# Kernel tuning notes

Measured on AMD Instinct MI355X. Metric: run time of the kernel, lower is better.

## Reference

```python
import jax, jax.numpy as jnp
import numpy as np

N_NODES = 100000
N_EDGES = 1600000
NEG_SLOPE = 0.2


def gat_layer(x, edge_index, W, att_src, att_dst, bias, concat):
    """PyG-style GATConv (v1) with self-loops added, dropout=0."""
    N = x.shape[0]
    H, C = att_src.shape
    ar = jnp.arange(N)
    src = jnp.concatenate([edge_index[0], ar])  # add self-loops
    dst = jnp.concatenate([edge_index[1], ar])
    h = (x @ W).reshape(N, H, C)                # [N,H,C]
    a_src = jnp.sum(h * att_src[None], axis=-1)  # [N,H]
    a_dst = jnp.sum(h * att_dst[None], axis=-1)  # [N,H]
    e = jax.nn.leaky_relu(a_src[src] + a_dst[dst], NEG_SLOPE)  # [E,H]
    # segment softmax over destination nodes
    m = jax.ops.segment_max(e, dst, num_segments=N)
    e = jnp.exp(e - m[dst])
    s = jax.ops.segment_sum(e, dst, num_segments=N)
    alpha = e / (s[dst] + 1e-16)                # [E,H]
    msg = h[src] * alpha[:, :, None]            # [E,H,C]
    out = jax.ops.segment_sum(msg, dst, num_segments=N)  # [N,H,C]
    if concat:
        out = out.reshape(N, H * C)
    else:
        out = out.mean(axis=1)
    return out + bias


def prelu(x, a):
    return jnp.where(x >= 0, x, a * x)


def setup_inputs() -> dict:
    key = jax.random.key(0)
    ks = jax.random.split(key, 12)
    def g(k, shape, fan):
        return jax.random.normal(k, shape, dtype=jnp.float32) * (1.0 / np.sqrt(fan))
    x = jax.random.normal(ks[0], (N_NODES, 256), dtype=jnp.float32)
    edge_index = jax.random.randint(ks[1], (2, N_EDGES), 0, N_NODES, dtype=jnp.int64 if jax.config.read('jax_enable_x64') else jnp.int32)
    return {
        'x': x,
        'edge_index': edge_index,
        'W1': g(ks[2], (256, 64), 256), 'as1': g(ks[3], (8, 8), 8), 'ad1': g(ks[4], (8, 8), 8), 'b1': jnp.zeros((64,), jnp.float32),
        'W2': g(ks[5], (320, 64), 320), 'as2': g(ks[6], (8, 8), 8), 'ad2': g(ks[7], (8, 8), 8), 'b2': jnp.zeros((64,), jnp.float32),
        'W3': g(ks[8], (64, 128), 64), 'as3': g(ks[9], (8, 16), 16), 'ad3': g(ks[10], (8, 16), 16), 'b3': jnp.zeros((16,), jnp.float32),
        'p1': jnp.full((1,), 0.25, jnp.float32), 'p2': jnp.full((1,), 0.25, jnp.float32),
    }


def reference(x, edge_index, W1, as1, ad1, b1, W2, as2, ad2, b2, W3, as3, ad3, b3, p1, p2):
    h = gat_layer(x, edge_index, W1, as1, ad1, b1, concat=True)
    h = prelu(h, p1)
    h = gat_layer(jnp.concatenate([x, h], axis=1), edge_index, W2, as2, ad2, b2, concat=True)
    h = prelu(h, p2)
    h = gat_layer(h, edge_index, W3, as3, ad3, b3, concat=False)
    return jax.nn.log_softmax(h, axis=1)
```

## Files before the change

kernel.cpp:

```cpp
#include <hip/hip_runtime.h>
#include <hip/hip_bf16.h>
#include <stdint.h>

typedef unsigned short u16;
typedef __attribute__((ext_vector_type(8))) short short8;
typedef __attribute__((ext_vector_type(8))) __bf16 bf16x8;
typedef __attribute__((ext_vector_type(4))) float f32x4;
typedef __attribute__((ext_vector_type(4))) float fv4;

#define DEV static __device__ __forceinline__

DEV float bf2f(u16 u) { uint32_t i = ((uint32_t)u) << 16; float f; __builtin_memcpy(&f, &i, 4); return f; }
DEV u16 f2bf(float f) {
    uint32_t i; __builtin_memcpy(&i, &f, 4);
    uint32_t r = i + 0x7FFFu + ((i >> 16) & 1u);
    return (u16)(r >> 16);
}
DEV float lo16f(uint32_t u) { uint32_t i = u << 16; float f; __builtin_memcpy(&f, &i, 4); return f; }
DEV float hi16f(uint32_t u) { uint32_t i = u & 0xFFFF0000u; float f; __builtin_memcpy(&f, &i, 4); return f; }
DEV uint32_t pack2(float a, float b) { return (uint32_t)f2bf(a) | ((uint32_t)f2bf(b) << 16); }
DEV float lrelu(float x) { return x >= 0.f ? x : 0.2f * x; }

#define CHK 4096
#define BN2SH 10
#define BN2 1024

__global__ __launch_bounds__(256) void k_cvt(const float* __restrict__ in, u16* __restrict__ out, int n4) {
    int i = blockIdx.x * 256 + threadIdx.x;
    if (i < n4) {
        fv4 v = __builtin_nontemporal_load((const fv4*)in + i);
        uint64_t o = (uint64_t)f2bf(v.x) | ((uint64_t)f2bf(v.y) << 16)
                   | ((uint64_t)f2bf(v.z) << 32) | ((uint64_t)f2bf(v.w) << 48);
        __builtin_nontemporal_store(o, (uint64_t*)out + i);
    }
}

__global__ __launch_bounds__(256) void k_wt(const float* __restrict__ W, u16* __restrict__ out, int K, int M) {
    int i = blockIdx.x * 256 + threadIdx.x;
    int nko = K >> 3;
    int total = (M >> 6) * 64 * nko;
    if (i >= total) return;
    int c = i % nko;
    int m = (i / nko) & 63;
    int cb = i / (nko * 64);
    const float* wp = W + (size_t)(c * 8) * M + cb * 64 + m;
    uint64_t w0 = (uint64_t)f2bf(wp[0])
                | ((uint64_t)f2bf(wp[(size_t)M]) << 16)
                | ((uint64_t)f2bf(wp[(size_t)2 * M]) << 32)
                | ((uint64_t)f2bf(wp[(size_t)3 * M]) << 48);
    uint64_t w1 = (uint64_t)f2bf(wp[(size_t)4 * M])
                | ((uint64_t)f2bf(wp[(size_t)5 * M]) << 16)
                | ((uint64_t)f2bf(wp[(size_t)6 * M]) << 32)
                | ((uint64_t)f2bf(wp[(size_t)7 * M]) << 48);
    uint64_t* d = (uint64_t*)out + (size_t)i * 2;
    d[0] = w0; d[1] = w1;
}

__global__ __launch_bounds__(256) void k_hist(const int* __restrict__ dst, int* __restrict__ hist,
                                              int NBUK, int nbp, int E) {
    __shared__ int h[BN2];
    int tid = threadIdx.x;
    for (int i = tid; i < NBUK; i += 256) h[i] = 0;
    __syncthreads();
    int b0 = blockIdx.x * CHK;
    int jend = b0 + CHK < E ? b0 + CHK : E;
    for (int j = b0 + tid; j < jend; j += 256)
        atomicAdd(&h[dst[j] >> BN2SH], 1);
    __syncthreads();
    for (int i = tid; i < NBUK; i += 256) hist[i * nbp + blockIdx.x] = h[i];
}

__global__ void k_scanpart(const int* __restrict__ deg, int* __restrict__ bsum, int n) {
    __shared__ int buf[1024];
    int tid = threadIdx.x;
    int i = blockIdx.x * 1024 + tid;
    int v = (i < n) ? deg[i] : 0;
    buf[tid] = v; __syncthreads();
    for (int d = 512; d > 0; d >>= 1) {
        if (tid < d) buf[tid] += buf[tid + d];
        __syncthreads();
    }
    if (tid == 0) bsum[blockIdx.x] = buf[0];
}

__global__ void k_scanbsum(int* bsum, int nb) {
    if (threadIdx.x == 0) {
        int run = 0;
        for (int b = 0; b < nb; ++b) { int t = bsum[b]; bsum[b] = run; run += t; }
    }
}

__global__ void k_scanonly(const int* __restrict__ in, const int* __restrict__ bsum,
                           int* __restrict__ out, int n) {
    __shared__ int buf[1024];
    int tid = threadIdx.x;
    int i = blockIdx.x * 1024 + tid;
    int v = (i < n) ? in[i] : 0;
    buf[tid] = v; __syncthreads();
    for (int d = 1; d < 1024; d <<= 1) {
        int t = (tid >= d) ? buf[tid - d] : 0;
        __syncthreads();
        buf[tid] += t;
        __syncthreads();
    }
    if (i < n) out[i] = buf[tid] - v + bsum[blockIdx.x];
}

__global__ __launch_bounds__(256) void k_part(const int* __restrict__ src, const int* __restrict__ dst,
                                              const int* __restrict__ scanned, int* __restrict__ stage,
                                              int NBUK, int nbp, int E) {
    __shared__ int cur[BN2];
    int tid = threadIdx.x;
    for (int i = tid; i < NBUK; i += 256) cur[i] = scanned[i * nbp + blockIdx.x];
    __syncthreads();
    int b0 = blockIdx.x * CHK;
    int jend = b0 + CHK < E ? b0 + CHK : E;
    for (int j = b0 + tid; j < jend; j += 256) {
        int d = dst[j];
        int p = atomicAdd(&cur[d >> BN2SH], 1);
        stage[p] = src[j] | ((d & (BN2 - 1)) << 17);
    }
}

__global__ __launch_bounds__(256) void k_csr(const int* __restrict__ stage, const int* __restrict__ scanned,
                                             int* __restrict__ off, int* __restrict__ srt,
                                             int NBUK, int nbp, int N, int E) {
    __shared__ int deg[BN2];
    __shared__ int ex[BN2];
    __shared__ int tsum[256];
    int tid = threadIdx.x, b = blockIdx.x;
    int base = b << BN2SH;
    int s0 = scanned[b * nbp];
    int s1 = (b + 1 < NBUK) ? scanned[(b + 1) * nbp] : E;
    for (int i = tid; i < BN2; i += 256) deg[i] = 0;
    __syncthreads();
    for (int j = s0 + tid; j < s1; j += 256) atomicAdd(&deg[(uint32_t)stage[j] >> 17], 1);
    __syncthreads();
    int t4 = tid * 4;
    int d0 = deg[t4], d1 = deg[t4 + 1], d2 = deg[t4 + 2], d3 = deg[t4 + 3];
    int tot = d0 + d1 + d2 + d3;
    tsum[tid] = tot; __syncthreads();
    for (int d = 1; d < 256; d <<= 1) {
        int t = (tid >= d) ? tsum[tid - d] : 0;
        __syncthreads();
        tsum[tid] += t;
        __syncthreads();
    }
    int ebase = tsum[tid] - tot;
    ex[t4] = ebase; ex[t4 + 1] = ebase + d0; ex[t4 + 2] = ebase + d0 + d1; ex[t4 + 3] = ebase + d0 + d1 + d2;
    __syncthreads();
    for (int i = tid; i < BN2; i += 256) { int n = base + i; if (n < N) off[n] = s0 + ex[i]; }
    if (b == 0 && tid == 0) off[N] = E;
    __syncthreads();
    for (int j = s0 + tid; j < s1; j += 256) {
        int sd = stage[j];
        int p = atomicAdd(&ex[(uint32_t)sd >> 17], 1);
        srt[s0 + p] = sd & 0x1FFFF;
    }
}

__global__ __launch_bounds__(256) void gemm_k(const u16* __restrict__ A1, int K1,
                                              const u16* __restrict__ A2, int K2,
                                              const u16* __restrict__ wbt, int M,
                                              u16* __restrict__ out, int N,
                                              const float* __restrict__ ats, const float* __restrict__ atd,
                                              float* __restrict__ a_src, float* __restrict__ a_dst, int hs) {
    __shared__ u16 wt2[40][64][8];
    const int K = K1 + K2;
    const int nc = K >> 3;
    const int tid = threadIdx.x;
    const int n0 = blockIdx.x * 64;
    const int cb = blockIdx.y * 64;

    const u16* wB = wbt + (size_t)cb * K;
    for (int p = tid; p < (nc << 6); p += 256) {
        int c = p >> 6, m = p & 63;
        *(int4*)&wt2[c][m][0] = *(const int4*)(wB + (size_t)m * K + c * 8);
    }
    __syncthreads();

    const int wv = tid >> 6, lane = tid & 63;
    const int quad = lane >> 4, r = lane & 15;
    f32x4 acc[4];
#pragma unroll
    for (int ct = 0; ct < 4; ++ct) acc[ct] = (f32x4){0.f, 0.f, 0.f, 0.f};

    int arow = n0 + wv * 16 + r;
    int ar = arow < N ? arow : N - 1;
    const u16* rowA1 = A1 + (size_t)ar * K1;
    const u16* rowA2 = A2 ? (A2 + (size_t)ar * K2 - K1) : rowA1;

    const int nit = K >> 5;
    for (int it = 0; it < nit; ++it) {
        int kk = (it << 5) + quad * 8;
        const u16* ap = (kk < K1) ? (rowA1 + kk) : (rowA2 + kk);
        bf16x8 a = __builtin_bit_cast(bf16x8, *(const short8*)ap);
        int cbase = it << 2;
#pragma unroll
        for (int ct = 0; ct < 4; ++ct) {
            bf16x8 b = __builtin_bit_cast(bf16x8, *(const short8*)&wt2[cbase + quad][ct * 16 + r][0]);
            acc[ct] = __builtin_amdgcn_mfma_f32_16x16x32_bf16(a, b, acc[ct], 0, 0, 0);
        }
    }

    const int rmask = (1 << hs) - 1;
#pragma unroll
    for (int ct = 0; ct < 4; ++ct) {
        int col = cb + ct * 16 + r;
        float as_c = ats[col];
        float ad_c = atd[col];
#pragma unroll
        for (int rg = 0; rg < 4; ++rg) {
            int grow = n0 + wv * 16 + quad * 4 + rg;
            float p = acc[ct][rg];
            if (grow < N) out[(size_t)grow * M + col] = f2bf(p);
            float ps = p * as_c;
            float pd = p * ad_c;
            ps += __shfl_xor(ps, 1); pd += __shfl_xor(pd, 1);
            ps += __shfl_xor(ps, 2); pd += __shfl_xor(pd, 2);
            ps += __shfl_xor(ps, 4); pd += __shfl_xor(pd, 4);
            if (rmask == 15) { ps += __shfl_xor(ps, 8); pd += __shfl_xor(pd, 8); }
            if ((r & rmask) == 0 && grow < N) {
                int head = col >> hs;
                a_src[grow * 8 + head] = ps;
                a_dst[grow * 8 + head] = pd;
            }
        }
    }
}

__global__ __launch_bounds__(256) void agg12(const u16* __restrict__ g,
                                             const float* __restrict__ a_src, const float* __restrict__ a_dst,
                                             const int* __restrict__ off, const int* __restrict__ srt,
                                             const float* __restrict__ bias, const float* __restrict__ pslope,
                                             u16* __restrict__ hout, int N) {
    int tid = threadIdx.x;
    int lane32 = tid & 31;
    int node = blockIdx.x * 8 + (tid >> 5);
    int nd = node < N ? node : N - 1;
    int lane16 = lane32 & 15;
    int sub    = lane32 >> 4;
    int hg     = lane16 >> 1;
    int hw     = lane32 & 7;
    int e4     = lane32 >> 3;
    const char* gb = (const char*)g;

    float ad_acc = a_dst[nd * 8 + hg];
    float ad_w   = a_dst[nd * 8 + hw];
    float ws = __expf(lrelu(a_src[nd * 8 + hg] + ad_acc));
    float m0 = (sub == 0) ? ws : 0.f;
    uint2 gs = *(const uint2*)(gb + ((size_t)nd << 7) + lane16 * 8);
    float s = m0;
    float acc0 = m0 * lo16f(gs.x), acc1 = m0 * hi16f(gs.x);
    float acc2 = m0 * lo16f(gs.y), acc3 = m0 * hi16f(gs.y);

    int jb = off[nd], je = off[nd + 1];
    int addrH = (tid & 32) * 4;
    int addrS = addrH + sub * 32;
    int addrW = addrS + hg * 4;
    int laneoff = lane16 * 8;

    int idx = 0; float asv = 0.f;
    if (jb < je) {
        int jc = jb + e4; jc = jc < je ? jc : je - 1;
        idx = srt[jc];
        asv = a_src[idx * 8 + hw];
    }
    for (int j = jb; j < je; j += 4) {
        float w = __expf(lrelu(asv + ad_w));
        w = (j + e4 < je) ? w : 0.f;
        int wi = __builtin_bit_cast(int, w);
        int jn = j + 4 + e4; jn = jn < je ? jn : je - 1;
        int idx_n = srt[jn];
        float as_n = a_src[idx_n * 8 + hw];

        int sv0 = __builtin_amdgcn_ds_bpermute(addrS,      idx);
        int wb0 = __builtin_amdgcn_ds_bpermute(addrW,      wi);
        int sv1 = __builtin_amdgcn_ds_bpermute(addrS + 64, idx);
        int wb1 = __builtin_amdgcn_ds_bpermute(addrW + 64, wi);
        uint2 g0 = *(const uint2*)(gb + (((uint32_t)sv0 << 7) + laneoff));
        uint2 g1 = *(const uint2*)(gb + (((uint32_t)sv1 << 7) + laneoff));
        float wv0 = __builtin_bit_cast(float, wb0);
        float wv1 = __builtin_bit_cast(float, wb1);
        s += wv0;
        acc0 += wv0 * lo16f(g0.x); acc1 += wv0 * hi16f(g0.x);
        acc2 += wv0 * lo16f(g0.y); acc3 += wv0 * hi16f(g0.y);
        s += wv1;
        acc0 += wv1 * lo16f(g1.x); acc1 += wv1 * hi16f(g1.x);
        acc2 += wv1 * lo16f(g1.y); acc3 += wv1 * hi16f(g1.y);
        idx = idx_n; asv = as_n;
    }
    s    += __shfl_xor(s,    16);
    acc0 += __shfl_xor(acc0, 16); acc1 += __shfl_xor(acc1, 16);
    acc2 += __shfl_xor(acc2, 16); acc3 += __shfl_xor(acc3, 16);
    if (node < N && sub == 0) {
        float r = 1.f / (s + 1e-16f);
        fv4 bv = *(const fv4*)(bias + lane16 * 4);
        float p = pslope[0];
        float v0 = acc0 * r + bv.x; v0 = v0 >= 0.f ? v0 : p * v0;
        float v1 = acc1 * r + bv.y; v1 = v1 >= 0.f ? v1 : p * v1;
        float v2 = acc2 * r + bv.z; v2 = v2 >= 0.f ? v2 : p * v2;
        float v3 = acc3 * r + bv.w; v3 = v3 >= 0.f ? v3 : p * v3;
        uint2 o; o.x = pack2(v0, v1); o.y = pack2(v2, v3);
        *(uint2*)((char*)hout + ((size_t)node << 7) + lane16 * 8) = o;
    }
}

__global__ __launch_bounds__(256) void agg3(const u16* __restrict__ g,
                                            const float* __restrict__ a_src, const float* __restrict__ a_dst,
                                            const int* __restrict__ off, const int* __restrict__ srt,
                                            const float* __restrict__ b3, float* __restrict__ out, int N) {
    int tid = threadIdx.x;
    int lane = tid & 63;
    int node = blockIdx.x * 4 + (tid >> 6);
    int nd = node < N ? node : N - 1;
    int lane32 = lane & 31;
    int sub = lane >> 5;
    int hg = lane32 >> 2;
    int hw = lane & 7;
    int e8 = lane >> 3;
    const char* gb = (const char*)g;

    float ad_acc = a_dst[nd * 8 + hg];
    float ad_w   = a_dst[nd * 8 + hw];
    float ws = __expf(lrelu(a_src[nd * 8 + hg] + ad_acc));
    float m0 = (sub == 0) ? ws : 0.f;
    uint2 gs = *(const uint2*)(gb + ((size_t)nd << 8) + lane32 * 8);
    float s = m0;
    float acc0 = m0 * lo16f(gs.x), acc1 = m0 * hi16f(gs.x);
    float acc2 = m0 * lo16f(gs.y), acc3 = m0 * hi16f(gs.y);

    int jb = off[nd], je = off[nd + 1];
    int addrS = sub * 32;
    int addrW = addrS + hg * 4;
    int laneoff = lane32 * 8;

    int idx = 0; float asv = 0.f;
    if (jb < je) {
        int jc = jb + e8; jc = jc < je ? jc : je - 1;
        idx = srt[jc];
        asv = a_src[idx * 8 + hw];
    }
    for (int j = jb; j < je; j += 8) {
        float w = __expf(lrelu(asv + ad_w));
        w = (j + e8 < je) ? w : 0.f;
        int wi = __builtin_bit_cast(int, w);
        int jn = j + 8 + e8; jn = jn < je ? jn : je - 1;
        int idx_n = srt[jn];
        float as_n = a_src[idx_n * 8 + hw];
#pragma unroll
        for (int t = 0; t < 4; ++t) {
            int sv = __builtin_amdgcn_ds_bpermute(addrS + t * 64, idx);
            int wb = __builtin_amdgcn_ds_bpermute(addrW + t * 64, wi);
            uint2 gv = *(const uint2*)(gb + (((uint32_t)sv << 8) + laneoff));
            float wf = __builtin_bit_cast(float, wb);
            s += wf;
            acc0 += wf * lo16f(gv.x); acc1 += wf * hi16f(gv.x);
            acc2 += wf * lo16f(gv.y); acc3 += wf * hi16f(gv.y);
        }
        idx = idx_n; asv = as_n;
    }
    s    += __shfl_xor(s,    32);
    acc0 += __shfl_xor(acc0, 32); acc1 += __shfl_xor(acc1, 32);
    acc2 += __shfl_xor(acc2, 32); acc3 += __shfl_xor(acc3, 32);
    float r = 1.f / (s + 1e-16f);
    acc0 *= r; acc1 *= r; acc2 *= r; acc3 *= r;
#pragma unroll
    for (int d = 4; d <= 16; d <<= 1) {
        acc0 += __shfl_xor(acc0, d); acc1 += __shfl_xor(acc1, d);
        acc2 += __shfl_xor(acc2, d); acc3 += __shfl_xor(acc3, d);
    }
    fv4 bv = *(const fv4*)(b3 + (lane32 & 3) * 4);
    float v0 = acc0 * 0.125f + bv.x;
    float v1 = acc1 * 0.125f + bv.y;
    float v2 = acc2 * 0.125f + bv.z;
    float v3 = acc3 * 0.125f + bv.w;
    float m = fmaxf(fmaxf(v0, v1), fmaxf(v2, v3));
    m = fmaxf(m, __shfl_xor(m, 1)); m = fmaxf(m, __shfl_xor(m, 2));
    float se = __expf(v0 - m) + __expf(v1 - m) + __expf(v2 - m) + __expf(v3 - m);
    se += __shfl_xor(se, 1); se += __shfl_xor(se, 2);
    float lg = __logf(se);
    if (node < N && lane < 4) {
        float4 o;
        o.x = v0 - m - lg; o.y = v1 - m - lg; o.z = v2 - m - lg; o.w = v3 - m - lg;
        *(float4*)(out + (size_t)node * 16 + lane * 4) = o;
    }
}

extern "C" void kernel_launch(void* const* d_in, const int* in_sizes, int n_in,
                              void* d_out, int out_size, void* d_ws, size_t ws_size,
                              hipStream_t stream) {
    (void)n_in; (void)out_size; (void)ws_size;
    const float* x  = (const float*)d_in[0];
    const int* ei   = (const int*)d_in[1];
    const float* W1 = (const float*)d_in[2];
    const float* as1 = (const float*)d_in[3];
    const float* ad1 = (const float*)d_in[4];
    const float* b1  = (const float*)d_in[5];
    const float* W2  = (const float*)d_in[6];
    const float* as2 = (const float*)d_in[7];
    const float* ad2 = (const float*)d_in[8];
    const float* b2  = (const float*)d_in[9];
    const float* W3  = (const float*)d_in[10];
    const float* as3 = (const float*)d_in[11];
    const float* ad3 = (const float*)d_in[12];
    const float* b3  = (const float*)d_in[13];
    const float* p1  = (const float*)d_in[14];
    const float* p2  = (const float*)d_in[15];
    const int N = in_sizes[0] / 256;
    const int E = in_sizes[1] / 2;
    const int NBUK = (N + BN2 - 1) >> BN2SH;
    const int nbp = (E + CHK - 1) / CHK;
    const int nsc = NBUK * nbp;

    char* ws = (char*)d_ws;
    size_t o = 0;
    auto alloc = [&](size_t bytes) { void* p = ws + o; o = (o + bytes + 255) & ~(size_t)255; return p; };
    int* off     = (int*)alloc((size_t)(N + 1) * 4);
    int* bsum    = (int*)alloc(4096);
    int* hist    = (int*)alloc((size_t)nsc * 4);
    int* scanned = (int*)alloc((size_t)nsc * 4);
    int* srt     = (int*)alloc((size_t)E * 4);
    int* stage   = (int*)alloc((size_t)E * 4);
    u16* xb      = (u16*)alloc((size_t)N * 256 * 2);
    u16* g       = (u16*)alloc((size_t)N * 128 * 2);
    float* a_src = (float*)alloc((size_t)N * 8 * 4);
    float* a_dst = (float*)alloc((size_t)N * 8 * 4);
    u16* h1      = (u16*)alloc((size_t)N * 64 * 2);
    u16* h2      = (u16*)alloc((size_t)N * 64 * 2);
    u16* wb1     = (u16*)alloc((size_t)256 * 64 * 2);
    u16* wb2     = (u16*)alloc((size_t)320 * 64 * 2);
    u16* wb3     = (u16*)alloc((size_t)64 * 128 * 2);

    int n4 = N * 256 / 4;
    k_cvt<<<(n4 + 255) / 256, 256, 0, stream>>>(x, xb, n4);

    k_wt<<<(256 * 64 / 8 + 255) / 256, 256, 0, stream>>>(W1, wb1, 256, 64);
    k_wt<<<(320 * 64 / 8 + 255) / 256, 256, 0, stream>>>(W2, wb2, 320, 64);
    k_wt<<<(64 * 128 / 8 + 255) / 256, 256, 0, stream>>>(W3, wb3, 64, 128);

    k_hist<<<nbp, 256, 0, stream>>>(ei + E, hist, NBUK, nbp, E);
    int nS = (nsc + 1023) / 1024;
    k_scanpart<<<nS, 1024, 0, stream>>>(hist, bsum, nsc);
    k_scanbsum<<<1, 64, 0, stream>>>(bsum, nS);
    k_scanonly<<<nS, 1024, 0, stream>>>(hist, bsum, scanned, nsc);
    k_part<<<nbp, 256, 0, stream>>>(ei, ei + E, scanned, stage, NBUK, nbp, E);
    k_csr<<<NBUK, 256, 0, stream>>>(stage, scanned, off, srt, NBUK, nbp, N, E);

    int nb64 = (N + 63) / 64;
    int nb4 = (N + 3) / 4;
    int nb8 = (N + 7) / 8;

    gemm_k<<<dim3(nb64, 1), 256, 0, stream>>>(xb, 256, (const u16*)nullptr, 0, wb1, 64, g, N,
                                              as1, ad1, a_src, a_dst, 3);
    agg12<<<nb8, 256, 0, stream>>>(g, a_src, a_dst, off, srt, b1, p1, h1, N);

    gemm_k<<<dim3(nb64, 1), 256, 0, stream>>>(xb, 256, h1, 64, wb2, 64, g, N,
                                              as2, ad2, a_src, a_dst, 3);
    agg12<<<nb8, 256, 0, stream>>>(g, a_src, a_dst, off, srt, b2, p2, h2, N);

    gemm_k<<<dim3(nb64, 2), 256, 0, stream>>>(h2, 64, (const u16*)nullptr, 0, wb3, 128, g, N,
                                              as3, ad3, a_src, a_dst, 4);
    agg3<<<nb4, 256, 0, stream>>>(g, a_src, a_dst, off, srt, b3, (float*)d_out, N);
}
```

Baseline: 538.8 us.

## Merge prologue and partition/GEMM launches into fused multi-role kernels, template GEMM on K

Histogram, weight conversion and x conversion now run in one multi-role kernel, and the bucket partition runs alongside the first GEMM in another, with blocks choosing their role by block index. The separate block-sum scan kernel is dropped; each scan block sums the preceding block totals itself. The GEMM is templated on K so its inner loop fully unrolls and its shared tile is sized to K. The aim is to remove launch overhead and let independent work overlap. The cost is mixed-role blocks, and in the merged partition/GEMM kernel every block reserves the full 32 KB GEMM shared tile, which may lower occupancy for the partition blocks.

Result: faster. 505.7 us (-6.2%).

```diff
diff --git a/kernel.cpp b/kernel.cpp
--- a/kernel.cpp
+++ b/kernel.cpp
@@ -25,18 +25,7 @@
 #define BN2SH 10
 #define BN2 1024
 
-__global__ __launch_bounds__(256) void k_cvt(const float* __restrict__ in, u16* __restrict__ out, int n4) {
-    int i = blockIdx.x * 256 + threadIdx.x;
-    if (i < n4) {
-        fv4 v = __builtin_nontemporal_load((const fv4*)in + i);
-        uint64_t o = (uint64_t)f2bf(v.x) | ((uint64_t)f2bf(v.y) << 16)
-                   | ((uint64_t)f2bf(v.z) << 32) | ((uint64_t)f2bf(v.w) << 48);
-        __builtin_nontemporal_store(o, (uint64_t*)out + i);
-    }
-}
-
-__global__ __launch_bounds__(256) void k_wt(const float* __restrict__ W, u16* __restrict__ out, int K, int M) {
-    int i = blockIdx.x * 256 + threadIdx.x;
+DEV void wt_elem(const float* __restrict__ W, u16* __restrict__ out, int K, int M, int i) {
     int nko = K >> 3;
     int total = (M >> 6) * 64 * nko;
     if (i >= total) return;
@@ -56,18 +45,41 @@
     d[0] = w0; d[1] = w1;
 }
 
-__global__ __launch_bounds__(256) void k_hist(const int* __restrict__ dst, int* __restrict__ hist,
-                                              int NBUK, int nbp, int E) {
+__global__ __launch_bounds__(256) void k_pro(
+    const float* __restrict__ x, u16* __restrict__ xb, int n4,
+    const float* __restrict__ W1, u16* __restrict__ wb1,
+    const float* __restrict__ W2, u16* __restrict__ wb2,
+    const float* __restrict__ W3, u16* __restrict__ wb3,
+    const int* __restrict__ dst, int* __restrict__ hist,
+    int NBUK, int nbp, int E) {
     __shared__ int h[BN2];
+    int bid = blockIdx.x;
     int tid = threadIdx.x;
-    for (int i = tid; i < NBUK; i += 256) h[i] = 0;
-    __syncthreads();
-    int b0 = blockIdx.x * CHK;
-    int jend = b0 + CHK < E ? b0 + CHK : E;
-    for (int j = b0 + tid; j < jend; j += 256)
-        atomicAdd(&h[dst[j] >> BN2SH], 1);
-    __syncthreads();
-    for (int i = tid; i < NBUK; i += 256) hist[i * nbp + blockIdx.x] = h[i];
+    if (bid < nbp) {
+        for (int i = tid; i < NBUK; i += 256) h[i] = 0;
+        __syncthreads();
+        int b0 = bid * CHK;
+        int jend = b0 + CHK < E ? b0 + CHK : E;
+        for (int j = b0 + tid; j < jend; j += 256)
+            atomicAdd(&h[dst[j] >> BN2SH], 1);
+        __syncthreads();
+        for (int i = tid; i < NBUK; i += 256) hist[i * nbp + bid] = h[i];
+        return;
+    }
+    bid -= nbp;
+    if (bid < 8)  { wt_elem(W1, wb1, 256, 64, bid * 256 + tid); return; }
+    bid -= 8;
+    if (bid < 10) { wt_elem(W2, wb2, 320, 64, bid * 256 + tid); return; }
+    bid -= 10;
+    if (bid < 4)  { wt_elem(W3, wb3, 64, 128, bid * 256 + tid); return; }
+    bid -= 4;
+    int i = bid * 256 + tid;
+    if (i < n4) {
+        fv4 v = __builtin_nontemporal_load((const fv4*)x + i);
+        uint64_t o = (uint64_t)f2bf(v.x) | ((uint64_t)f2bf(v.y) << 16)
+                   | ((uint64_t)f2bf(v.z) << 32) | ((uint64_t)f2bf(v.w) << 48);
+        __builtin_nontemporal_store(o, (uint64_t*)xb + i);
+    }
 }
 
 __global__ void k_scanpart(const int* __restrict__ deg, int* __restrict__ bsum, int n) {
@@ -83,17 +95,16 @@
     if (tid == 0) bsum[blockIdx.x] = buf[0];
 }
 
-__global__ void k_scanbsum(int* bsum, int nb) {
-    if (threadIdx.x == 0) {
-        int run = 0;
-        for (int b = 0; b < nb; ++b) { int t = bsum[b]; bsum[b] = run; run += t; }
-    }
-}
-
 __global__ void k_scanonly(const int* __restrict__ in, const int* __restrict__ bsum,
                            int* __restrict__ out, int n) {
     __shared__ int buf[1024];
+    __shared__ int base;
     int tid = threadIdx.x;
+    if (tid == 0) {
+        int run = 0;
+        for (int b = 0; b < (int)blockIdx.x; ++b) run += bsum[b];
+        base = run;
+    }
     int i = blockIdx.x * 1024 + tid;
     int v = (i < n) ? in[i] : 0;
     buf[tid] = v; __syncthreads();
@@ -103,23 +114,117 @@
         buf[tid] += t;
         __syncthreads();
     }
-    if (i < n) out[i] = buf[tid] - v + bsum[blockIdx.x];
-}
-
-__global__ __launch_bounds__(256) void k_part(const int* __restrict__ src, const int* __restrict__ dst,
-                                              const int* __restrict__ scanned, int* __restrict__ stage,
-                                              int NBUK, int nbp, int E) {
-    __shared__ int cur[BN2];
-    int tid = threadIdx.x;
-    for (int i = tid; i < NBUK; i += 256) cur[i] = scanned[i * nbp + blockIdx.x];
+    if (i < n) out[i] = buf[tid] - v + base;
+}
+
+template<int TK>
+DEV void gemm_body(int bx, int by,
+                   const u16* __restrict__ A1, int K1,
+                   const u16* __restrict__ A2,
+                   const u16* __restrict__ wbt, int M,
+                   u16* __restrict__ out, int N,
+                   const float* __restrict__ ats, const float* __restrict__ atd,
+                   float* __restrict__ a_src, float* __restrict__ a_dst, int hs,
+                   u16 (*wt2)[64][8]) {
+    const int nc = TK >> 3;
+    const int tid = threadIdx.x;
+    const int n0 = bx * 64;
+    const int cb = by * 64;
+
+    const u16* wB = wbt + (size_t)cb * TK;
+    for (int p = tid; p < (nc << 6); p += 256) {
+        int c = p >> 6, m = p & 63;
+        *(int4*)&wt2[c][m][0] = *(const int4*)(wB + (size_t)m * TK + c * 8);
+    }
     __syncthreads();
-    int b0 = blockIdx.x * CHK;
-    int jend = b0 + CHK < E ? b0 + CHK : E;
-    for (int j = b0 + tid; j < jend; j += 256) {
-        int d = dst[j];
-        int p = atomicAdd(&cur[d >> BN2SH], 1);
-        stage[p] = src[j] | ((d & (BN2 - 1)) << 17);
-    }
+
+    const int wv = tid >> 6, lane = tid & 63;
+    const int quad = lane >> 4, r = lane & 15;
+    f32x4 acc[4];
+#pragma unroll
+    for (int ct = 0; ct < 4; ++ct) acc[ct] = (f32x4){0.f, 0.f, 0.f, 0.f};
+
+    int arow = n0 + wv * 16 + r;
+    int ar = arow < N ? arow : N - 1;
+    const u16* rowA1 = A1 + (size_t)ar * K1;
+    const u16* rowA2 = A2 ? (A2 + (size_t)ar * (TK - K1) - K1) : rowA1;
+
+    const int nit = TK >> 5;
+#pragma unroll
+    for (int it = 0; it < nit; ++it) {
+        int kk = (it << 5) + quad * 8;
+        const u16* ap = (kk < K1) ? (rowA1 + kk) : (rowA2 + kk);
+        bf16x8 a = __builtin_bit_cast(bf16x8, *(const short8*)ap);
+        int cbase = it << 2;
+#pragma unroll
+        for (int ct = 0; ct < 4; ++ct) {
+            bf16x8 b = __builtin_bit_cast(bf16x8, *(const short8*)&wt2[cbase + quad][ct * 16 + r][0]);
+            acc[ct] = __builtin_amdgcn_mfma_f32_16x16x32_bf16(a, b, acc[ct], 0, 0, 0);
+        }
+    }
+
+    const int rmask = (1 << hs) - 1;
+#pragma unroll
+    for (int ct = 0; ct < 4; ++ct) {
+        int col = cb + ct * 16 + r;
+        float as_c = ats[col];
+        float ad_c = atd[col];
+#pragma unroll
+        for (int rg = 0; rg < 4; ++rg) {
+            int grow = n0 + wv * 16 + quad * 4 + rg;
+            float p = acc[ct][rg];
+            if (grow < N) out[(size_t)grow * M + col] = f2bf(p);
+            float ps = p * as_c;
+            float pd = p * ad_c;
+            ps += __shfl_xor(ps, 1); pd += __shfl_xor(pd, 1);
+            ps += __shfl_xor(ps, 2); pd += __shfl_xor(pd, 2);
+            ps += __shfl_xor(ps, 4); pd += __shfl_xor(pd, 4);
+            if (rmask == 15) { ps += __shfl_xor(ps, 8); pd += __shfl_xor(pd, 8); }
+            if ((r & rmask) == 0 && grow < N) {
+                int head = col >> hs;
+                a_src[grow * 8 + head] = ps;
+                a_dst[grow * 8 + head] = pd;
+            }
+        }
+    }
+}
+
+template<int TK>
+__global__ __launch_bounds__(256) void gemm_k(const u16* __restrict__ A1, int K1,
+                                              const u16* __restrict__ A2,
+                                              const u16* __restrict__ wbt, int M,
+                                              u16* __restrict__ out, int N,
+                                              const float* __restrict__ ats, const float* __restrict__ atd,
+                                              float* __restrict__ a_src, float* __restrict__ a_dst, int hs) {
+    __shared__ u16 wt2[TK / 8][64][8];
+    gemm_body<TK>(blockIdx.x, blockIdx.y, A1, K1, A2, wbt, M, out, N, ats, atd, a_src, a_dst, hs, wt2);
+}
+
+__global__ __launch_bounds__(256) void k_pg(
+    const int* __restrict__ src, const int* __restrict__ dst,
+    const int* __restrict__ scanned, int* __restrict__ stage, int NBUK, int nbp, int E,
+    const u16* __restrict__ A1, const u16* __restrict__ wbt,
+    u16* __restrict__ out, int N,
+    const float* __restrict__ ats, const float* __restrict__ atd,
+    float* __restrict__ a_src, float* __restrict__ a_dst) {
+    __shared__ u16 wt2[32][64][8];
+    int bid = blockIdx.x;
+    if (bid < nbp) {
+        int* cur = (int*)wt2;
+        int tid = threadIdx.x;
+        for (int i = tid; i < NBUK; i += 256) cur[i] = scanned[i * nbp + bid];
+        __syncthreads();
+        int b0 = bid * CHK;
+        int jend = b0 + CHK < E ? b0 + CHK : E;
+        for (int j = b0 + tid; j < jend; j += 256) {
+            int d = dst[j];
+            int p = atomicAdd(&cur[d >> BN2SH], 1);
+            stage[p] = src[j] | ((d & (BN2 - 1)) << 17);
+        }
+        return;
+    }
+    gemm_body<256>(bid - nbp, 0, A1, 256, (const u16*)nullptr, wbt, 64, out, N,
+                   ats, atd, a_src, a_dst, 3, wt2);
 }
 
 __global__ __launch_bounds__(256) void k_csr(const int* __restrict__ stage, const int* __restrict__ scanned,
@@ -156,76 +261,6 @@
         int sd = stage[j];
         int p = atomicAdd(&ex[(uint32_t)sd >> 17], 1);
         srt[s0 + p] = sd & 0x1FFFF;
-    }
-}
-
-__global__ __launch_bounds__(256) void gemm_k(const u16* __restrict__ A1, int K1,
-                                              const u16* __restrict__ A2, int K2,
-                                              const u16* __restrict__ wbt, int M,
-                                              u16* __restrict__ out, int N,
-                                              const float* __restrict__ ats, const float* __restrict__ atd,
-                                              float* __restrict__ a_src, float* __restrict__ a_dst, int hs) {
-    __shared__ u16 wt2[40][64][8];
-    const int K = K1 + K2;
-    const int nc = K >> 3;
-    const int tid = threadIdx.x;
-    const int n0 = blockIdx.x * 64;
-    const int cb = blockIdx.y * 64;
-
-    const u16* wB = wbt + (size_t)cb * K;
-    for (int p = tid; p < (nc << 6); p += 256) {
-        int c = p >> 6, m = p & 63;
-        *(int4*)&wt2[c][m][0] = *(const int4*)(wB + (size_t)m * K + c * 8);
-    }
-    __syncthreads();
-
-    const int wv = tid >> 6, lane = tid & 63;
-    const int quad = lane >> 4, r = lane & 15;
-    f32x4 acc[4];
-#pragma unroll
-    for (int ct = 0; ct < 4; ++ct) acc[ct] = (f32x4){0.f, 0.f, 0.f, 0.f};
-
-    int arow = n0 + wv * 16 + r;
-    int ar = arow < N ? arow : N - 1;
-    const u16* rowA1 = A1 + (size_t)ar * K1;
-    const u16* rowA2 = A2 ? (A2 + (size_t)ar * K2 - K1) : rowA1;
-
-    const int nit = K >> 5;
-    for (int it = 0; it < nit; ++it) {
-        int kk = (it << 5) + quad * 8;
-        const u16* ap = (kk < K1) ? (rowA1 + kk) : (rowA2 + kk);
-        bf16x8 a = __builtin_bit_cast(bf16x8, *(const short8*)ap);
-        int cbase = it << 2;
-#pragma unroll
-        for (int ct = 0; ct < 4; ++ct) {
-            bf16x8 b = __builtin_bit_cast(bf16x8, *(const short8*)&wt2[cbase + quad][ct * 16 + r][0]);
-            acc[ct] = __builtin_amdgcn_mfma_f32_16x16x32_bf16(a, b, acc[ct], 0, 0, 0);
-        }
-    }
-
-    const int rmask = (1 << hs) - 1;
-#pragma unroll
-    for (int ct = 0; ct < 4; ++ct) {
-        int col = cb + ct * 16 + r;
-        float as_c = ats[col];
-        float ad_c = atd[col];
-#pragma unroll
-        for (int rg = 0; rg < 4; ++rg) {
-            int grow = n0 + wv * 16 + quad * 4 + rg;
-            float p = acc[ct][rg];
-            if (grow < N) out[(size_t)grow * M + col] = f2bf(p);
-            float ps = p * as_c;
-            float pd = p * ad_c;
-            ps += __shfl_xor(ps, 1); pd += __shfl_xor(pd, 1);
-            ps += __shfl_xor(ps, 2); pd += __shfl_xor(pd, 2);
-            ps += __shfl_xor(ps, 4); pd += __shfl_xor(pd, 4);
-            if (rmask == 15) { ps += __shfl_xor(ps, 8); pd += __shfl_xor(pd, 8); }
-            if ((r & rmask) == 0 && grow < N) {
-                int head = col >> hs;
-                a_src[grow * 8 + head] = ps;
-                a_dst[grow * 8 + head] = pd;
-            }
-        }
     }
 }
 
@@ -433,33 +468,30 @@
     u16* wb3     = (u16*)alloc((size_t)64 * 128 * 2);
 
     int n4 = N * 256 / 4;
-    k_cvt<<<(n4 + 255) / 256, 256, 0, stream>>>(x, xb, n4);
-
-    k_wt<<<(256 * 64 / 8 + 255) / 256, 256, 0, stream>>>(W1, wb1, 256, 64);
-    k_wt<<<(320 * 64 / 8 + 255) / 256, 256, 0, stream>>>(W2, wb2, 320, 64);
-    k_wt<<<(64 * 128 / 8 + 255) / 256, 256, 0, stream>>>(W3, wb3, 64, 128);
-
-    k_hist<<<nbp, 256, 0, stream>>>(ei + E, hist, NBUK, nbp, E);
+    int ncvt = (n4 + 255) / 256;
+
+    k_pro<<<nbp + 22 + ncvt, 256, 0, stream>>>(x, xb, n4, W1, wb1, W2, wb2, W3, wb3,
+                                               ei + E, hist, NBUK, nbp, E);
+
     int nS = (nsc + 1023) / 1024;
     k_scanpart<<<nS, 1024, 0, stream>>>(hist, bsum, nsc);
-    k_scanbsum<<<1, 64, 0, stream>>>(bsum, nS);
     k_scanonly<<<nS, 1024, 0, stream>>>(hist, bsum, scanned, nsc);
-    k_part<<<nbp, 256, 0, stream>>>(ei, ei + E, scanned, stage, NBUK, nbp, E);
-    k_csr<<<NBUK, 256, 0, stream>>>(stage, scanned, off, srt, NBUK, nbp, N, E);
 
     int nb64 = (N + 63) / 64;
     int nb4 = (N + 3) / 4;
     int nb8 = (N + 7) / 8;
 
-    gemm_k<<<dim3(nb64, 1), 256, 0, stream>>>(xb, 256, (const u16*)nullptr, 0, wb1, 64, g, N,
-                                              as1, ad1, a_src, a_dst, 3);
+    k_pg<<<nbp + nb64, 256, 0, stream>>>(ei, ei + E, scanned, stage, NBUK, nbp, E,
+                                         xb, wb1, g, N, as1, ad1, a_src, a_dst);
+    k_csr<<<NBUK, 256, 0, stream>>>(stage, scanned, off, srt, NBUK, nbp, N, E);
+
     agg12<<<nb8, 256, 0, stream>>>(g, a_src, a_dst, off, srt, b1, p1, h1, N);
 
-    gemm_k<<<dim3(nb64, 1), 256, 0, stream>>>(xb, 256, h1, 64, wb2, 64, g, N,
-                                              as2, ad2, a_src, a_dst, 3);
+    gemm_k<320><<<dim3(nb64, 1), 256, 0, stream>>>(xb, 256, h1, wb2, 64, g, N,
+                                                   as2, ad2, a_src, a_dst, 3);
     agg12<<<nb8, 256, 0, stream>>>(g, a_src, a_dst, off, srt, b2, p2, h2, N);
 
-    gemm_k<<<dim3(nb64, 2), 256, 0, stream>>>(h2, 64, (const u16*)nullptr, 0, wb3, 128, g, N,
-                                              as3, ad3, a_src, a_dst, 4);
+    gemm_k<64><<<dim3(nb64, 2), 256, 0, stream>>>(h2, 64, (const u16*)nullptr, wb3, 128, g, N,
+                                                  as3, ad3, a_src, a_dst, 4);
     agg3<<<nb4, 256, 0, stream>>>(g, a_src, a_dst, off, srt, b3, (float*)d_out, N);
 }
```
